# Kernel tuning notes

Hardware: AMD Instinct MI355X
Metric: run time of the kernel (lower is better)

Reference implementation:

```python
import jax, jax.numpy as jnp
import numpy as np

B, C, H, W = 32, 256, 32, 32

def conv1x1(x, w, b):
    # x: [b,c,h,w], w: [out,in], b: [out]  (1x1 conv == per-pixel linear)
    return jnp.einsum('bchw,oc->bohw', x, w) + b[None, :, None, None]

def setup_inputs() -> dict:
    key = jax.random.key(0)
    ks = jax.random.split(key, 16)
    scale = 1.0 / np.sqrt(C)
    def wgt(k):
        return jax.random.normal(k, (C, C), dtype=jnp.float32) * scale
    def bia(k):
        return jax.random.normal(k, (C,), dtype=jnp.float32) * 0.01
    return {
        'x1': jax.random.normal(ks[0], (B, C, H, W), dtype=jnp.float32),
        'x2': jax.random.normal(ks[1], (B, C, H, W), dtype=jnp.float32),
        'wq1': wgt(ks[2]), 'bq1': bia(ks[3]),
        'wk': wgt(ks[4]), 'bk': bia(ks[5]),
        'wv': wgt(ks[6]), 'bv': bia(ks[7]),
        'wq2': wgt(ks[8]), 'bq2': bia(ks[9]),
        'wps': wgt(ks[10]), 'bps': bia(ks[11]),
        'wpc': wgt(ks[12]), 'bpc': bia(ks[13]),
    }

def reference(x1, x2, wq1, bq1, wk, bk, wv, bv, wq2, bq2, wps, bps, wpc, bpc):
    b, c, h, w = x1.shape
    hw = h * w
    inv_sqrt_c = c ** (-0.5)

    def tokens(t):  # [b,c,h,w] -> [b,hw,c]  (matches permute(0,2,3,1).view)
        return jnp.transpose(t, (0, 2, 3, 1)).reshape(b, hw, c)

    q1 = tokens(conv1x1(x1, wq1, bq1))
    k = tokens(conv1x1(x1, wk, bk))
    v = tokens(conv1x1(x1, wv, bv))  # [b,hw,c]

    # self-attention scores: [b, q_tokens, k_tokens]
    w1 = jnp.einsum('bqc,bkc->bqk', q1, k) * inv_sqrt_c
    a1 = jax.nn.softmax(w1, axis=-1)
    h1 = jnp.einsum('bqk,bkc->bqc', a1, v)  # [b,hw,c]
    h1 = jnp.transpose(h1, (0, 2, 1)).reshape(b, c, h, w)
    h1 = conv1x1(h1, wps, bps)

    # cross-attention: q from x2, shared k/v from x1, scores added
    q2 = tokens(conv1x1(x2, wq2, bq2))
    w2 = jnp.einsum('bqc,bkc->bqk', q2, k) * inv_sqrt_c
    a12 = jax.nn.softmax(w1 + w2, axis=-1)
    h12 = jnp.einsum('bqk,bkc->bqc', a12, v)
    h12 = jnp.transpose(h12, (0, 2, 1)).reshape(b, c, h, w)
    h12 = conv1x1(h12, wpc, bpc)

    return (x1 + h1, x1 + h12)
```

## Files before the change

kernel.cpp:

```cpp
#include <hip/hip_runtime.h>
#include <math.h>

#define Bn 32
#define Cn 256
#define Pn 1024
#define Tn (Bn * Pn * Cn)

typedef __bf16 bf16x8 __attribute__((ext_vector_type(8)));
typedef float  f32x4  __attribute__((ext_vector_type(4)));
typedef unsigned short u16;
typedef u16 u16x8 __attribute__((ext_vector_type(8)));

#define XT1o ((size_t)0)
#define XT2o ((size_t)1 * Tn)
#define Q1o  ((size_t)2 * Tn)
#define Ko   ((size_t)3 * Tn)
#define VTo  ((size_t)4 * Tn)
#define Q2o  ((size_t)5 * Tn)
#define H1o  ((size_t)6 * Tn)
#define H12o ((size_t)7 * Tn)
#define WBo  ((size_t)8 * Tn)

__device__ __forceinline__ u16 f2b(float f) {
    union { float f; unsigned u; } c; c.f = f;
    return (u16)((c.u + 0x7FFFu + ((c.u >> 16) & 1u)) >> 16);
}

__global__ __launch_bounds__(256) void cvt_kernel(
    const float* __restrict__ x1, const float* __restrict__ x2,
    const float* __restrict__ wq1, const float* __restrict__ wk,
    const float* __restrict__ wv,  const float* __restrict__ wq2,
    const float* __restrict__ wps, const float* __restrict__ wpc,
    u16* __restrict__ ws16)
{
    const int z = blockIdx.z;
    const int tid = threadIdx.x;
    if (z >= 64) {
        const int widx = z - 64;
        const float* w = widx == 0 ? wq1 : widx == 1 ? wk : widx == 2 ? wv
                       : widx == 3 ? wq2 : widx == 4 ? wps : wpc;
        const int linear = blockIdx.x + 16 * blockIdx.y;
        const int e = linear * 1024 + tid * 4;
        float4 v = *(const float4*)&w[e];
        ushort4 o = make_ushort4(f2b(v.x), f2b(v.y), f2b(v.z), f2b(v.w));
        *(ushort4*)&ws16[WBo + (size_t)widx * 65536 + e] = o;
        return;
    }
    const int which = z >> 5, b = z & 31;
    const float* x = which ? x2 : x1;
    u16* xt = ws16 + (which ? XT2o : XT1o);
    const int p0 = blockIdx.x * 64, c0 = blockIdx.y * 64;
    __shared__ __align__(16) u16 T[64][80];
    #pragma unroll
    for (int i = 0; i < 4; i++) {
        int e = tid + i * 256;
        int c = e >> 4, p4 = e & 15;
        float4 v = *(const float4*)&x[((size_t)(b * Cn + c0 + c)) * Pn + p0 + p4 * 4];
        T[p4 * 4 + 0][c] = f2b(v.x);
        T[p4 * 4 + 1][c] = f2b(v.y);
        T[p4 * 4 + 2][c] = f2b(v.z);
        T[p4 * 4 + 3][c] = f2b(v.w);
    }
    __syncthreads();
    #pragma unroll
    for (int i = 0; i < 2; i++) {
        int e = tid + i * 256;
        int p = e >> 3, c8 = e & 7;
        u16x8 vv = *(const u16x8*)&T[p][c8 * 8];
        *(u16x8*)&xt[((size_t)(b * Pn + p0 + p)) * Cn + c0 + c8 * 8] = vv;
    }
}

__device__ __forceinline__ void gemm_core(
    const u16* __restrict__ Ab, const u16* __restrict__ Bb,
    u16* __restrict__ As, u16* __restrict__ Bs, f32x4 acc[16], int tid)
{
    const int wv = tid >> 6, lane = tid & 63;
    const int ln = lane & 15, quad = lane >> 4;
    const int wr = wv >> 1, wc = wv & 1;
    const int srow = tid >> 3, sch = tid & 7;
    const int pos = sch ^ (srow & 7);

    u16x8 apre[4], bpre[4];
    #pragma unroll
    for (int i = 0; i < 4; i++) {
        int r = srow + 32 * i;
        apre[i] = *(const u16x8*)&Ab[(size_t)r * 256 + sch * 8];
        bpre[i] = *(const u16x8*)&Bb[(size_t)r * 256 + sch * 8];
    }

    for (int k0 = 0; k0 < 256; k0 += 64) {
        __syncthreads();
        #pragma unroll
        for (int i = 0; i < 4; i++) {
            int r = srow + 32 * i;
            *(u16x8*)&As[r * 64 + pos * 8] = apre[i];
            *(u16x8*)&Bs[r * 64 + pos * 8] = bpre[i];
        }
        __syncthreads();
        if (k0 < 192) {
            #pragma unroll
            for (int i = 0; i < 4; i++) {
                int r = srow + 32 * i;
                apre[i] = *(const u16x8*)&Ab[(size_t)r * 256 + (k0 + 64) + sch * 8];
                bpre[i] = *(const u16x8*)&Bb[(size_t)r * 256 + (k0 + 64) + sch * 8];
            }
        }
        bf16x8 af[4][2], bf[4][2];
        #pragma unroll
        for (int i = 0; i < 4; i++) {
            int row = wr * 64 + i * 16 + ln;
            #pragma unroll
            for (int kc = 0; kc < 2; kc++) {
                int p = (kc * 4 + quad) ^ (row & 7);
                af[i][kc] = *(const bf16x8*)&As[row * 64 + p * 8];
            }
        }
        #pragma unroll
        for (int j = 0; j < 4; j++) {
            int row = wc * 64 + j * 16 + ln;
            #pragma unroll
            for (int kc = 0; kc < 2; kc++) {
                int p = (kc * 4 + quad) ^ (row & 7);
                bf[j][kc] = *(const bf16x8*)&Bs[row * 64 + p * 8];
            }
        }
        #pragma unroll
        for (int kc = 0; kc < 2; kc++)
            #pragma unroll
            for (int i = 0; i < 4; i++)
                #pragma unroll
                for (int j = 0; j < 4; j++)
                    acc[i * 4 + j] = __builtin_amdgcn_mfma_f32_16x16x32_bf16(
                        af[i][kc], bf[j][kc], acc[i * 4 + j], 0, 0, 0);
    }
}

__global__ __launch_bounds__(256) void proj_kernel(
    u16* __restrict__ ws16,
    const float* __restrict__ bq1, const float* __restrict__ bk,
    const float* __restrict__ bq2, const float* __restrict__ bv)
{
    __shared__ __align__(16) u16 As[128 * 64];
    __shared__ __align__(16) u16 Bs[128 * 64];
    const int tid = threadIdx.x;
    const int mat = blockIdx.y;
    const int wv = tid >> 6, lane = tid & 63;
    const int ln = lane & 15, quad = lane >> 4;
    const int wr = wv >> 1, wc = wv & 1;

    f32x4 acc[16];
    #pragma unroll
    for (int t = 0; t < 16; t++) acc[t] = (f32x4){0.f, 0.f, 0.f, 0.f};

    if (mat < 3) {
        const int m_tile = blockIdx.x >> 1, n_tile = blockIdx.x & 1;
        const size_t xtoff = (mat == 2) ? XT2o : XT1o;
        const int widx = (mat == 0) ? 0 : (mat == 1) ? 1 : 3;
        const float* bias = (mat == 0) ? bq1 : (mat == 1) ? bk : bq2;
        const float scale = (mat == 1) ? 1.0f : 0.0625f;
        u16* out = ws16 + ((mat == 0) ? Q1o : (mat == 1) ? Ko : Q2o);

        const u16* Ab = ws16 + xtoff + (size_t)m_tile * 128 * 256;
        const u16* Bb = ws16 + WBo + (size_t)widx * 65536 + (size_t)n_tile * 128 * 256;
        gemm_core(Ab, Bb, As, Bs, acc, tid);

        const int m0 = m_tile * 128;
        #pragma unroll
        for (int j = 0; j < 4; j++) {
            const int ncol = n_tile * 128 + wc * 64 + j * 16 + ln;
            const float bj = bias[ncol];
            #pragma unroll
            for (int i = 0; i < 4; i++) {
                const int mr = m0 + wr * 64 + i * 16 + quad * 4;
                #pragma unroll
                for (int r = 0; r < 4; r++)
                    out[(size_t)(mr + r) * 256 + ncol] =
                        f2b((acc[i * 4 + j][r] + bj) * scale);
            }
        }
    } else {
        const int b = blockIdx.x >> 4;
        const int o_tile = (blockIdx.x >> 3) & 1;
        const int p_tile = blockIdx.x & 7;
        const u16* Ab = ws16 + WBo + (size_t)2 * 65536 + (size_t)o_tile * 128 * 256;
        const u16* Bb = ws16 + XT1o + ((size_t)b * Pn + p_tile * 128) * 256;
        gemm_core(Ab, Bb, As, Bs, acc, tid);

        u16* vt = ws16 + VTo + (size_t)b * Cn * Pn;
        #pragma unroll
        for (int i = 0; i < 4; i++) {
            #pragma unroll
            for (int r = 0; r < 4; r++) {
                const int orow = o_tile * 128 + wr * 64 + i * 16 + quad * 4 + r;
                const float bo = bv[orow];
                #pragma unroll
                for (int j = 0; j < 4; j++) {
                    const int pcol = p_tile * 128 + wc * 64 + j * 16 + ln;
                    vt[(size_t)orow * Pn + pcol] = f2b(acc[i * 4 + j][r] + bo);
                }
            }
        }
    }
}

__global__ __launch_bounds__(256, 2) void attn_kernel(u16* __restrict__ ws16)
{
    const u16* Q1 = ws16 + Q1o;
    const u16* Kg = ws16 + Ko;
    const u16* Vt = ws16 + VTo;
    const u16* Q2 = ws16 + Q2o;

    __shared__ __align__(16) u16 Klds[32 * 256];
    __shared__ __align__(16) u16 Vtlds[256 * 32];
    __shared__ __align__(16) u16 Plds[4 * 2 * 16 * 40];

    const int b    = blockIdx.y;
    const int q0   = blockIdx.x * 64;
    const int tid  = threadIdx.x;
    const int wid  = tid >> 6;
    const int lane = tid & 63;
    const int ln   = lane & 15;
    const int quad = lane >> 4;
    u16* Pw = Plds + wid * (2 * 16 * 40);

    const size_t qrow = (size_t)(b * Pn + q0 + wid * 16 + ln) * Cn;
    bf16x8 qa1[8], qa2[8];
    #pragma unroll
    for (int ch = 0; ch < 8; ch++) {
        qa1[ch] = *(const bf16x8*)&Q1[qrow + ch * 32 + quad * 8];
        qa2[ch] = *(const bf16x8*)&Q2[qrow + ch * 32 + quad * 8];
    }

    f32x4 acc1[16], acc12[16];
    #pragma unroll
    for (int t = 0; t < 16; t++) {
        acc1[t] = (f32x4){0.f, 0.f, 0.f, 0.f};
        acc12[t] = (f32x4){0.f, 0.f, 0.f, 0.f};
    }
    float lp1[4] = {}, lp12[4] = {};

    const int tokK = tid >> 3, giK = tid & 7;
    const int cbV = tid >> 2, gvV = tid & 3;
    u16x8 kpre[4], vpre[4];

    {
        const size_t growK = (size_t)(b * Pn + 0 + tokK) * Cn;
        #pragma unroll
        for (int i = 0; i < 4; i++)
            kpre[i] = *(const u16x8*)&Kg[growK + (size_t)(8 * i + (giK ^ (tokK & 7))) * 8];
        #pragma unroll
        for (int i = 0; i < 4; i++) {
            int cl = cbV + 64 * i;
            vpre[i] = *(const u16x8*)&Vt[((size_t)(b * Cn + cl)) * Pn + 0 + gvV * 8];
        }
    }

    for (int kt = 0; kt < 32; kt++) {
        __syncthreads();

        #pragma unroll
        for (int i = 0; i < 4; i++)
            *(u16x8*)&Klds[tokK * 256 + (8 * i + giK) * 8] = kpre[i];
        #pragma unroll
        for (int i = 0; i < 4; i++) {
            int cl = cbV + 64 * i;
            int gp = gvV ^ (cl & 3);
            *(u16x8*)&Vtlds[cl * 32 + gp * 8] = vpre[i];
        }
        __syncthreads();

        if (kt < 31) {
            const int k0n = (kt + 1) * 32;
            const size_t growK = (size_t)(b * Pn + k0n + tokK) * Cn;
            #pragma unroll
            for (int i = 0; i < 4; i++)
                kpre[i] = *(const u16x8*)&Kg[growK + (size_t)(8 * i + (giK ^ (tokK & 7))) * 8];
            #pragma unroll
            for (int i = 0; i < 4; i++) {
                int cl = cbV + 64 * i;
                vpre[i] = *(const u16x8*)&Vt[((size_t)(b * Cn + cl)) * Pn + k0n + gvV * 8];
            }
        }

        float s1v[2][4], s2v[2][4];
        #pragma unroll
        for (int st = 0; st < 2; st++) {
            f32x4 s1 = (f32x4){0.f, 0.f, 0.f, 0.f};
            f32x4 s2 = (f32x4){0.f, 0.f, 0.f, 0.f};
            #pragma unroll
            for (int ch = 0; ch < 8; ch++) {
                bf16x8 kb = *(const bf16x8*)
                    &Klds[(st * 16 + ln) * 256 + (((ch * 4 + quad) ^ (ln & 7))) * 8];
                s1 = __builtin_amdgcn_mfma_f32_16x16x32_bf16(qa1[ch], kb, s1, 0, 0, 0);
                s2 = __builtin_amdgcn_mfma_f32_16x16x32_bf16(qa2[ch], kb, s2, 0, 0, 0);
            }
            #pragma unroll
            for (int r = 0; r < 4; r++) { s1v[st][r] = s1[r]; s2v[st][r] = s2[r]; }
        }

        #pragma unroll
        for (int st = 0; st < 2; st++)
            #pragma unroll
            for (int r = 0; r < 4; r++) {
                float p1 = __expf(s1v[st][r]);
                float p12 = p1 * __expf(s2v[st][r]);
                lp1[r] += p1;
                lp12[r] += p12;
                int row = quad * 4 + r, col = st * 16 + ln;
                Pw[row * 40 + col]            = f2b(p1);
                Pw[16 * 40 + row * 40 + col]  = f2b(p12);
            }

        bf16x8 pa1 = *(const bf16x8*)&Pw[ln * 40 + quad * 8];
        bf16x8 pa2 = *(const bf16x8*)&Pw[16 * 40 + ln * 40 + quad * 8];
        #pragma unroll
        for (int t = 0; t < 16; t++) {
            bf16x8 vb = *(const bf16x8*)
                &Vtlds[(t * 16 + ln) * 32 + (quad ^ (ln & 3)) * 8];
            acc1[t]  = __builtin_amdgcn_mfma_f32_16x16x32_bf16(pa1, vb, acc1[t], 0, 0, 0);
            acc12[t] = __builtin_amdgcn_mfma_f32_16x16x32_bf16(pa2, vb, acc12[t], 0, 0, 0);
        }
    }

    u16* H1 = ws16 + H1o;
    u16* H12 = ws16 + H12o;
    #pragma unroll
    for (int r = 0; r < 4; r++) {
        float l1 = lp1[r], l2 = lp12[r];
        l1 += __shfl_xor(l1, 1); l2 += __shfl_xor(l2, 1);
        l1 += __shfl_xor(l1, 2); l2 += __shfl_xor(l2, 2);
        l1 += __shfl_xor(l1, 4); l2 += __shfl_xor(l2, 4);
        l1 += __shfl_xor(l1, 8); l2 += __shfl_xor(l2, 8);
        float i1 = 1.f / l1, i2 = 1.f / l2;
        size_t rowb = (size_t)(b * Pn + q0 + wid * 16 + quad * 4 + r) * Cn;
        #pragma unroll
        for (int t = 0; t < 16; t++) {
            H1[rowb + t * 16 + ln]  = f2b(acc1[t][r] * i1);
            H12[rowb + t * 16 + ln] = f2b(acc12[t][r] * i2);
        }
    }
}

__global__ __launch_bounds__(256) void outproj_kernel(
    const float* __restrict__ x1,
    const float* __restrict__ bps, const float* __restrict__ bpc,
    const u16* __restrict__ ws16, float* __restrict__ outp)
{
    __shared__ __align__(16) u16 As[128 * 64];
    __shared__ __align__(16) u16 Bs[128 * 64];
    const int tid = threadIdx.x;
    const int o_tile = blockIdx.x >> 3, p_tile = blockIdx.x & 7;
    const int mat = blockIdx.y >> 5, b = blockIdx.y & 31;
    const int wv = tid >> 6, lane = tid & 63;
    const int ln = lane & 15, quad = lane >> 4;
    const int wr = wv >> 1, wc = wv & 1;

    f32x4 acc[16];
    #pragma unroll
    for (int t = 0; t < 16; t++) acc[t] = (f32x4){0.f, 0.f, 0.f, 0.f};

    const u16* Ab = ws16 + WBo + (size_t)(4 + mat) * 65536 + (size_t)o_tile * 128 * 256;
    const u16* Bb = ws16 + (mat ? H12o : H1o) + ((size_t)b * Pn + p_tile * 128) * 256;
    gemm_core(Ab, Bb, As, Bs, acc, tid);

    const float* bias = mat ? bpc : bps;
    float* out = outp + (size_t)mat * Tn;
    #pragma unroll
    for (int i = 0; i < 4; i++) {
        #pragma unroll
        for (int r = 0; r < 4; r++) {
            const int orow = o_tile * 128 + wr * 64 + i * 16 + quad * 4 + r;
            const float bo = bias[orow];
            #pragma unroll
            for (int j = 0; j < 4; j++) {
                const int pcol = p_tile * 128 + wc * 64 + j * 16 + ln;
                const size_t idx = ((size_t)b * Cn + orow) * Pn + pcol;
                out[idx] = x1[idx] + bo + acc[i * 4 + j][r];
            }
        }
    }
}

extern "C" void kernel_launch(void* const* d_in, const int* in_sizes, int n_in,
                              void* d_out, int out_size, void* d_ws, size_t ws_size,
                              hipStream_t stream)
{
    const float* x1  = (const float*)d_in[0];
    const float* x2  = (const float*)d_in[1];
    const float* wq1 = (const float*)d_in[2];
    const float* bq1 = (const float*)d_in[3];
    const float* wk  = (const float*)d_in[4];
    const float* bk  = (const float*)d_in[5];
    const float* wv  = (const float*)d_in[6];
    const float* bv  = (const float*)d_in[7];
    const float* wq2 = (const float*)d_in[8];
    const float* bq2 = (const float*)d_in[9];
    const float* wps = (const float*)d_in[10];
    const float* bps = (const float*)d_in[11];
    const float* wpc = (const float*)d_in[12];
    const float* bpc = (const float*)d_in[13];
    float* out = (float*)d_out;
    u16* ws16 = (u16*)d_ws;

    cvt_kernel<<<dim3(16, 4, 70), 256, 0, stream>>>(
        x1, x2, wq1, wk, wv, wq2, wps, wpc, ws16);
    proj_kernel<<<dim3(512, 4), 256, 0, stream>>>(ws16, bq1, bk, bq2, bv);
    attn_kernel<<<dim3(Pn / 64, Bn), 256, 0, stream>>>(ws16);
    outproj_kernel<<<dim3(16, 64), 256, 0, stream>>>(x1, bps, bpc, ws16, out);
}
```

Measured before the change: 300.4 us.

## Load V fragments directly from global, remap blocks for L2 locality, add MFMA priority

The attention kernel stops staging V^T tiles in LDS. Each wave now loads its V MFMA operands straight from global memory in four groups interleaved with the MFMAs, which cuts LDS traffic and LDS footprint. Block indices are remapped so that co-scheduled blocks spread across batches in a set pattern, meant to change L2/MALL reuse of K/V. s_setprio raises wave priority around MFMA bursts. The trade-off is that every wave redundantly fetches V from global/L2, four times per block, and more global-load latency is exposed inside the loop.

Result: slower. 553.9 us (+84.4%).

```diff
diff --git a/kernel.cpp b/kernel.cpp
--- a/kernel.cpp
+++ b/kernel.cpp
@@ -212,11 +212,12 @@
     const u16* Q2 = ws16 + Q2o;
 
     __shared__ __align__(16) u16 Klds[32 * 256];
-    __shared__ __align__(16) u16 Vtlds[256 * 32];
     __shared__ __align__(16) u16 Plds[4 * 2 * 16 * 40];
 
-    const int b    = blockIdx.y;
-    const int q0   = blockIdx.x * 64;
+    const int fid = blockIdx.x + (blockIdx.y << 4);
+    const int b   = ((fid & 7) << 2) | ((fid >> 3) & 3);
+    const int q0  = (fid >> 5) << 6;
+
     const int tid  = threadIdx.x;
     const int wid  = tid >> 6;
     const int lane = tid & 63;
@@ -241,53 +242,42 @@
     float lp1[4] = {}, lp12[4] = {};
 
     const int tokK = tid >> 3, giK = tid & 7;
-    const int cbV = tid >> 2, gvV = tid & 3;
-    u16x8 kpre[4], vpre[4];
-
+    u16x8 kpre[4];
     {
-        const size_t growK = (size_t)(b * Pn + 0 + tokK) * Cn;
+        const size_t growK = (size_t)(b * Pn + tokK) * Cn;
         #pragma unroll
         for (int i = 0; i < 4; i++)
             kpre[i] = *(const u16x8*)&Kg[growK + (size_t)(8 * i + (giK ^ (tokK & 7))) * 8];
-        #pragma unroll
-        for (int i = 0; i < 4; i++) {
-            int cl = cbV + 64 * i;
-            vpre[i] = *(const u16x8*)&Vt[((size_t)(b * Cn + cl)) * Pn + 0 + gvV * 8];
-        }
-    }
+    }
+
+    const size_t vbase = ((size_t)b * Cn + ln) * Pn + quad * 8;
 
     for (int kt = 0; kt < 32; kt++) {
+        const int k0 = kt * 32;
         __syncthreads();
 
         #pragma unroll
         for (int i = 0; i < 4; i++)
             *(u16x8*)&Klds[tokK * 256 + (8 * i + giK) * 8] = kpre[i];
-        #pragma unroll
-        for (int i = 0; i < 4; i++) {
-            int cl = cbV + 64 * i;
-            int gp = gvV ^ (cl & 3);
-            *(u16x8*)&Vtlds[cl * 32 + gp * 8] = vpre[i];
-        }
         __syncthreads();
 
         if (kt < 31) {
-            const int k0n = (kt + 1) * 32;
-            const size_t growK = (size_t)(b * Pn + k0n + tokK) * Cn;
+            const size_t growK = (size_t)(b * Pn + k0 + 32 + tokK) * Cn;
             #pragma unroll
             for (int i = 0; i < 4; i++)
                 kpre[i] = *(const u16x8*)&Kg[growK + (size_t)(8 * i + (giK ^ (tokK & 7))) * 8];
-            #pragma unroll
-            for (int i = 0; i < 4; i++) {
-                int cl = cbV + 64 * i;
-                vpre[i] = *(const u16x8*)&Vt[((size_t)(b * Cn + cl)) * Pn + k0n + gvV * 8];
-            }
-        }
-
-        float s1v[2][4], s2v[2][4];
+        }
+
+        bf16x8 vb0[4], vb1[4];
+        #pragma unroll
+        for (int i = 0; i < 4; i++)
+            vb0[i] = *(const bf16x8*)&Vt[vbase + (size_t)(i * 16) * Pn + k0];
+
         #pragma unroll
         for (int st = 0; st < 2; st++) {
             f32x4 s1 = (f32x4){0.f, 0.f, 0.f, 0.f};
             f32x4 s2 = (f32x4){0.f, 0.f, 0.f, 0.f};
+            __builtin_amdgcn_s_setprio(1);
             #pragma unroll
             for (int ch = 0; ch < 8; ch++) {
                 bf16x8 kb = *(const bf16x8*)
@@ -295,32 +285,59 @@
                 s1 = __builtin_amdgcn_mfma_f32_16x16x32_bf16(qa1[ch], kb, s1, 0, 0, 0);
                 s2 = __builtin_amdgcn_mfma_f32_16x16x32_bf16(qa2[ch], kb, s2, 0, 0, 0);
             }
-            #pragma unroll
-            for (int r = 0; r < 4; r++) { s1v[st][r] = s1[r]; s2v[st][r] = s2[r]; }
-        }
-
-        #pragma unroll
-        for (int st = 0; st < 2; st++)
+            __builtin_amdgcn_s_setprio(0);
+            if (st == 0) {
+                #pragma unroll
+                for (int i = 0; i < 4; i++)
+                    vb1[i] = *(const bf16x8*)&Vt[vbase + (size_t)((i + 4) * 16) * Pn + k0];
+            }
             #pragma unroll
             for (int r = 0; r < 4; r++) {
-                float p1 = __expf(s1v[st][r]);
-                float p12 = p1 * __expf(s2v[st][r]);
+                float p1 = __expf(s1[r]);
+                float p12 = p1 * __expf(s2[r]);
                 lp1[r] += p1;
                 lp12[r] += p12;
-                int row = quad * 4 + r, col = st * 16 + ln;
-                Pw[row * 40 + col]            = f2b(p1);
-                Pw[16 * 40 + row * 40 + col]  = f2b(p12);
-            }
+                const int row = quad * 4 + r, col = st * 16 + ln;
+                Pw[row * 40 + col]           = f2b(p1);
+                Pw[16 * 40 + row * 40 + col] = f2b(p12);
+            }
+        }
 
         bf16x8 pa1 = *(const bf16x8*)&Pw[ln * 40 + quad * 8];
         bf16x8 pa2 = *(const bf16x8*)&Pw[16 * 40 + ln * 40 + quad * 8];
-        #pragma unroll
-        for (int t = 0; t < 16; t++) {
-            bf16x8 vb = *(const bf16x8*)
-                &Vtlds[(t * 16 + ln) * 32 + (quad ^ (ln & 3)) * 8];
-            acc1[t]  = __builtin_amdgcn_mfma_f32_16x16x32_bf16(pa1, vb, acc1[t], 0, 0, 0);
-            acc12[t] = __builtin_amdgcn_mfma_f32_16x16x32_bf16(pa2, vb, acc12[t], 0, 0, 0);
-        }
+
+        __builtin_amdgcn_s_setprio(1);
+        #pragma unroll
+        for (int t = 0; t < 4; t++) {
+            acc1[t]  = __builtin_amdgcn_mfma_f32_16x16x32_bf16(pa1, vb0[t], acc1[t], 0, 0, 0);
+            acc12[t] = __builtin_amdgcn_mfma_f32_16x16x32_bf16(pa2, vb0[t], acc12[t], 0, 0, 0);
+        }
+        __builtin_amdgcn_s_setprio(0);
+        #pragma unroll
+        for (int i = 0; i < 4; i++)
+            vb0[i] = *(const bf16x8*)&Vt[vbase + (size_t)((i + 8) * 16) * Pn + k0];
+        __builtin_amdgcn_s_setprio(1);
+        #pragma unroll
+        for (int t = 4; t < 8; t++) {
+            acc1[t]  = __builtin_amdgcn_mfma_f32_16x16x32_bf16(pa1, vb1[t - 4], acc1[t], 0, 0, 0);
+            acc12[t] = __builtin_amdgcn_mfma_f32_16x16x32_bf16(pa2, vb1[t - 4], acc12[t], 0, 0, 0);
+        }
+        __builtin_amdgcn_s_setprio(0);
+        #pragma unroll
+        for (int i = 0; i < 4; i++)
+            vb1[i] = *(const bf16x8*)&Vt[vbase + (size_t)((i + 12) * 16) * Pn + k0];
+        __builtin_amdgcn_s_setprio(1);
+        #pragma unroll
+        for (int t = 8; t < 12; t++) {
+            acc1[t]  = __builtin_amdgcn_mfma_f32_16x16x32_bf16(pa1, vb0[t - 8], acc1[t], 0, 0, 0);
+            acc12[t] = __builtin_amdgcn_mfma_f32_16x16x32_bf16(pa2, vb0[t - 8], acc12[t], 0, 0, 0);
+        }
+        #pragma unroll
+        for (int t = 12; t < 16; t++) {
+            acc1[t]  = __builtin_amdgcn_mfma_f32_16x16x32_bf16(pa1, vb1[t - 12], acc1[t], 0, 0, 0);
+            acc12[t] = __builtin_amdgcn_mfma_f32_16x16x32_bf16(pa2, vb1[t - 12], acc12[t], 0, 0, 0);
+        }
+        __builtin_amdgcn_s_setprio(0);
     }
 
     u16* H1 = ws16 + H1o;
```

## Keep attention probabilities in registers via transposed MFMA and permlane swaps

Applied to the files above, without the earlier changes.

Swaps the MFMA operand order so score tiles come out transposed, with each lane holding one query row. The probabilities are packed to bf16 with v_cvt_pk_bf16 and rearranged into the PV A-operand layout using permlane32/16 swaps, so the per-tile LDS store, read-back and extra LDS buffer go away. Row sums become one scalar per lane, reduced across quads once at the end. Outputs are written as 4-wide vector stores. This relies on the gfx950 permlane swap instructions and on getting the fragment mapping exactly right.

New measurement: 357.9 us. +19.1%, slower.

```diff
diff --git a/kernel.cpp b/kernel.cpp
--- a/kernel.cpp
+++ b/kernel.cpp
@@ -9,6 +9,7 @@
 typedef __bf16 bf16x8 __attribute__((ext_vector_type(8)));
 typedef float  f32x4  __attribute__((ext_vector_type(4)));
 typedef unsigned short u16;
+typedef unsigned int u32;
 typedef u16 u16x8 __attribute__((ext_vector_type(8)));
 
 #define XT1o ((size_t)0)
@@ -24,6 +25,23 @@
 __device__ __forceinline__ u16 f2b(float f) {
     union { float f; unsigned u; } c; c.f = f;
     return (u16)((c.u + 0x7FFFu + ((c.u >> 16) & 1u)) >> 16);
+}
+
+__device__ __forceinline__ u32 cvt_pk_bf16(float lo, float hi) {
+    u32 r;
+    asm("v_cvt_pk_bf16_f32 %0, %1, %2" : "=v"(r) : "v"(lo), "v"(hi));
+    return r;
+}
+__device__ __forceinline__ void pl32swap(u32& x, u32& y) {
+    asm("v_permlane32_swap_b32 %0, %1" : "+v"(x), "+v"(y));
+}
+__device__ __forceinline__ void pl16swap(u32& x, u32& y) {
+    asm("v_permlane16_swap_b32 %0, %1" : "+v"(x), "+v"(y));
+}
+__device__ __forceinline__ bf16x8 pkfrag(u32 a, u32 b, u32 c, u32 d) {
+    union { u32 u[4]; bf16x8 v; } x;
+    x.u[0] = a; x.u[1] = b; x.u[2] = c; x.u[3] = d;
+    return x.v;
 }
 
 __global__ __launch_bounds__(256) void cvt_kernel(
@@ -213,7 +231,6 @@
 
     __shared__ __align__(16) u16 Klds[32 * 256];
     __shared__ __align__(16) u16 Vtlds[256 * 32];
-    __shared__ __align__(16) u16 Plds[4 * 2 * 16 * 40];
 
     const int b    = blockIdx.y;
     const int q0   = blockIdx.x * 64;
@@ -222,7 +239,6 @@
     const int lane = tid & 63;
     const int ln   = lane & 15;
     const int quad = lane >> 4;
-    u16* Pw = Plds + wid * (2 * 16 * 40);
 
     const size_t qrow = (size_t)(b * Pn + q0 + wid * 16 + ln) * Cn;
     bf16x8 qa1[8], qa2[8];
@@ -238,7 +254,7 @@
         acc1[t] = (f32x4){0.f, 0.f, 0.f, 0.f};
         acc12[t] = (f32x4){0.f, 0.f, 0.f, 0.f};
     }
-    float lp1[4] = {}, lp12[4] = {};
+    float lp1 = 0.f, lp12 = 0.f;
 
     const int tokK = tid >> 3, giK = tid & 7;
     const int cbV = tid >> 2, gvV = tid & 3;
@@ -283,7 +299,7 @@
             }
         }
 
-        float s1v[2][4], s2v[2][4];
+        u32 pk1[4], pk2[4];
         #pragma unroll
         for (int st = 0; st < 2; st++) {
             f32x4 s1 = (f32x4){0.f, 0.f, 0.f, 0.f};
@@ -292,53 +308,58 @@
             for (int ch = 0; ch < 8; ch++) {
                 bf16x8 kb = *(const bf16x8*)
                     &Klds[(st * 16 + ln) * 256 + (((ch * 4 + quad) ^ (ln & 7))) * 8];
-                s1 = __builtin_amdgcn_mfma_f32_16x16x32_bf16(qa1[ch], kb, s1, 0, 0, 0);
-                s2 = __builtin_amdgcn_mfma_f32_16x16x32_bf16(qa2[ch], kb, s2, 0, 0, 0);
-            }
-            #pragma unroll
-            for (int r = 0; r < 4; r++) { s1v[st][r] = s1[r]; s2v[st][r] = s2[r]; }
-        }
-
-        #pragma unroll
-        for (int st = 0; st < 2; st++)
+                s1 = __builtin_amdgcn_mfma_f32_16x16x32_bf16(kb, qa1[ch], s1, 0, 0, 0);
+                s2 = __builtin_amdgcn_mfma_f32_16x16x32_bf16(kb, qa2[ch], s2, 0, 0, 0);
+            }
+            float p1v[4], p2v[4];
             #pragma unroll
             for (int r = 0; r < 4; r++) {
-                float p1 = __expf(s1v[st][r]);
-                float p12 = p1 * __expf(s2v[st][r]);
-                lp1[r] += p1;
-                lp12[r] += p12;
-                int row = quad * 4 + r, col = st * 16 + ln;
-                Pw[row * 40 + col]            = f2b(p1);
-                Pw[16 * 40 + row * 40 + col]  = f2b(p12);
-            }
-
-        bf16x8 pa1 = *(const bf16x8*)&Pw[ln * 40 + quad * 8];
-        bf16x8 pa2 = *(const bf16x8*)&Pw[16 * 40 + ln * 40 + quad * 8];
+                float e1 = __expf(s1[r]);
+                float e12 = e1 * __expf(s2[r]);
+                lp1 += e1;
+                lp12 += e12;
+                p1v[r] = e1;
+                p2v[r] = e12;
+            }
+            pk1[st * 2 + 0] = cvt_pk_bf16(p1v[0], p1v[1]);
+            pk1[st * 2 + 1] = cvt_pk_bf16(p1v[2], p1v[3]);
+            pk2[st * 2 + 0] = cvt_pk_bf16(p2v[0], p2v[1]);
+            pk2[st * 2 + 1] = cvt_pk_bf16(p2v[2], p2v[3]);
+        }
+
+        pl32swap(pk1[0], pk1[2]); pl32swap(pk1[1], pk1[3]);
+        pl32swap(pk2[0], pk2[2]); pl32swap(pk2[1], pk2[3]);
+        pl16swap(pk1[0], pk1[2]); pl16swap(pk1[1], pk1[3]);
+        pl16swap(pk2[0], pk2[2]); pl16swap(pk2[1], pk2[3]);
+
+        bf16x8 pa1 = pkfrag(pk1[0], pk1[1], pk1[2], pk1[3]);
+        bf16x8 pa2 = pkfrag(pk2[0], pk2[1], pk2[2], pk2[3]);
+
         #pragma unroll
         for (int t = 0; t < 16; t++) {
             bf16x8 vb = *(const bf16x8*)
                 &Vtlds[(t * 16 + ln) * 32 + (quad ^ (ln & 3)) * 8];
-            acc1[t]  = __builtin_amdgcn_mfma_f32_16x16x32_bf16(pa1, vb, acc1[t], 0, 0, 0);
-            acc12[t] = __builtin_amdgcn_mfma_f32_16x16x32_bf16(pa2, vb, acc12[t], 0, 0, 0);
-        }
-    }
+            acc1[t]  = __builtin_amdgcn_mfma_f32_16x16x32_bf16(vb, pa1, acc1[t], 0, 0, 0);
+            acc12[t] = __builtin_amdgcn_mfma_f32_16x16x32_bf16(vb, pa2, acc12[t], 0, 0, 0);
+        }
+    }
+
+    lp1  += __shfl_xor(lp1, 16);  lp1  += __shfl_xor(lp1, 32);
+    lp12 += __shfl_xor(lp12, 16); lp12 += __shfl_xor(lp12, 32);
+    const float i1 = 1.f / lp1, i2 = 1.f / lp12;
 
     u16* H1 = ws16 + H1o;
     u16* H12 = ws16 + H12o;
-    #pragma unroll
-    for (int r = 0; r < 4; r++) {
-        float l1 = lp1[r], l2 = lp12[r];
-        l1 += __shfl_xor(l1, 1); l2 += __shfl_xor(l2, 1);
-        l1 += __shfl_xor(l1, 2); l2 += __shfl_xor(l2, 2);
-        l1 += __shfl_xor(l1, 4); l2 += __shfl_xor(l2, 4);
-        l1 += __shfl_xor(l1, 8); l2 += __shfl_xor(l2, 8);
-        float i1 = 1.f / l1, i2 = 1.f / l2;
-        size_t rowb = (size_t)(b * Pn + q0 + wid * 16 + quad * 4 + r) * Cn;
-        #pragma unroll
-        for (int t = 0; t < 16; t++) {
-            H1[rowb + t * 16 + ln]  = f2b(acc1[t][r] * i1);
-            H12[rowb + t * 16 + ln] = f2b(acc12[t][r] * i2);
-        }
+    const size_t rowb = (size_t)(b * Pn + q0 + wid * 16 + ln) * Cn;
+    #pragma unroll
+    for (int t = 0; t < 16; t++) {
+        ushort4 o1, o2;
+        o1.x = f2b(acc1[t][0] * i1);  o1.y = f2b(acc1[t][1] * i1);
+        o1.z = f2b(acc1[t][2] * i1);  o1.w = f2b(acc1[t][3] * i1);
+        o2.x = f2b(acc12[t][0] * i2); o2.y = f2b(acc12[t][1] * i2);
+        o2.z = f2b(acc12[t][2] * i2); o2.w = f2b(acc12[t][3] * i2);
+        *(ushort4*)&H1[rowb + t * 16 + quad * 4]  = o1;
+        *(ushort4*)&H12[rowb + t * 16 + quad * 4] = o2;
     }
 }
 
```

## Double-buffer K/V tiles in LDS to halve barriers in attention loop

Applied to the files above, without the earlier changes.

The attention kernel now keeps two LDS buffers each for the K and V^T tiles and alternates between them. While one buffer is being read by the MFMA compute, the next tile's prefetched registers are written into the other. This drops one __syncthreads per key tile and lets the LDS staging overlap with compute. LDS per block roughly doubles for K/V, which could reduce occupancy if the 2-blocks-per-CU target no longer fits.

Result: slower. 575.9 us (+91.7%).

```diff
diff --git a/kernel.cpp b/kernel.cpp
--- a/kernel.cpp
+++ b/kernel.cpp
@@ -211,8 +211,10 @@
     const u16* Vt = ws16 + VTo;
     const u16* Q2 = ws16 + Q2o;
 
-    __shared__ __align__(16) u16 Klds[32 * 256];
-    __shared__ __align__(16) u16 Vtlds[256 * 32];
+    __shared__ __align__(16) u16 K0lds[32 * 256];
+    __shared__ __align__(16) u16 K1lds[32 * 256];
+    __shared__ __align__(16) u16 V0lds[256 * 32];
+    __shared__ __align__(16) u16 V1lds[256 * 32];
     __shared__ __align__(16) u16 Plds[4 * 2 * 16 * 40];
 
     const int b    = blockIdx.y;
@@ -244,45 +246,29 @@
     const int cbV = tid >> 2, gvV = tid & 3;
     u16x8 kpre[4], vpre[4];
 
-    {
-        const size_t growK = (size_t)(b * Pn + 0 + tokK) * Cn;
+    auto loads = [&](int k0n) {
+        const size_t growK = (size_t)(b * Pn + k0n + tokK) * Cn;
         #pragma unroll
         for (int i = 0; i < 4; i++)
             kpre[i] = *(const u16x8*)&Kg[growK + (size_t)(8 * i + (giK ^ (tokK & 7))) * 8];
         #pragma unroll
         for (int i = 0; i < 4; i++) {
             int cl = cbV + 64 * i;
-            vpre[i] = *(const u16x8*)&Vt[((size_t)(b * Cn + cl)) * Pn + 0 + gvV * 8];
-        }
-    }
-
-    for (int kt = 0; kt < 32; kt++) {
-        __syncthreads();
-
+            vpre[i] = *(const u16x8*)&Vt[((size_t)(b * Cn + cl)) * Pn + k0n + gvV * 8];
+        }
+    };
+    auto stage = [&](u16* Kb, u16* Vb) {
         #pragma unroll
         for (int i = 0; i < 4; i++)
-            *(u16x8*)&Klds[tokK * 256 + (8 * i + giK) * 8] = kpre[i];
+            *(u16x8*)&Kb[tokK * 256 + (8 * i + giK) * 8] = kpre[i];
         #pragma unroll
         for (int i = 0; i < 4; i++) {
             int cl = cbV + 64 * i;
             int gp = gvV ^ (cl & 3);
-            *(u16x8*)&Vtlds[cl * 32 + gp * 8] = vpre[i];
-        }
-        __syncthreads();
-
-        if (kt < 31) {
-            const int k0n = (kt + 1) * 32;
-            const size_t growK = (size_t)(b * Pn + k0n + tokK) * Cn;
-            #pragma unroll
-            for (int i = 0; i < 4; i++)
-                kpre[i] = *(const u16x8*)&Kg[growK + (size_t)(8 * i + (giK ^ (tokK & 7))) * 8];
-            #pragma unroll
-            for (int i = 0; i < 4; i++) {
-                int cl = cbV + 64 * i;
-                vpre[i] = *(const u16x8*)&Vt[((size_t)(b * Cn + cl)) * Pn + k0n + gvV * 8];
-            }
-        }
-
+            *(u16x8*)&Vb[cl * 32 + gp * 8] = vpre[i];
+        }
+    };
+    auto compute = [&](const u16* Kb, const u16* Vb) {
         float s1v[2][4], s2v[2][4];
         #pragma unroll
         for (int st = 0; st < 2; st++) {
@@ -291,7 +277,7 @@
             #pragma unroll
             for (int ch = 0; ch < 8; ch++) {
                 bf16x8 kb = *(const bf16x8*)
-                    &Klds[(st * 16 + ln) * 256 + (((ch * 4 + quad) ^ (ln & 7))) * 8];
+                    &Kb[(st * 16 + ln) * 256 + (((ch * 4 + quad) ^ (ln & 7))) * 8];
                 s1 = __builtin_amdgcn_mfma_f32_16x16x32_bf16(qa1[ch], kb, s1, 0, 0, 0);
                 s2 = __builtin_amdgcn_mfma_f32_16x16x32_bf16(qa2[ch], kb, s2, 0, 0, 0);
             }
@@ -317,9 +303,27 @@
         #pragma unroll
         for (int t = 0; t < 16; t++) {
             bf16x8 vb = *(const bf16x8*)
-                &Vtlds[(t * 16 + ln) * 32 + (quad ^ (ln & 3)) * 8];
+                &Vb[(t * 16 + ln) * 32 + (quad ^ (ln & 3)) * 8];
             acc1[t]  = __builtin_amdgcn_mfma_f32_16x16x32_bf16(pa1, vb, acc1[t], 0, 0, 0);
             acc12[t] = __builtin_amdgcn_mfma_f32_16x16x32_bf16(pa2, vb, acc12[t], 0, 0, 0);
+        }
+    };
+
+    loads(0);
+    stage(K0lds, V0lds);
+    loads(32);
+    __syncthreads();
+
+    for (int i = 0; i < 16; i++) {
+        compute(K0lds, V0lds);
+        stage(K1lds, V1lds);
+        if (i < 15) loads((2 * i + 2) * 32);
+        __syncthreads();
+        compute(K1lds, V1lds);
+        if (i < 15) {
+            stage(K0lds, V0lds);
+            loads((2 * i + 3) * 32);
+            __syncthreads();
         }
     }
 
```
